# Performance work log

Hardware: AMD Instinct MI355X
Metric: run time of the kernel (lower is better)

The kernel has to match this reference:

```python
import jax, jax.numpy as jnp
import numpy as np

N_NODES = 40000
N_EDGES = 640000
D_IN = 128
D_OUT = 128


def setup_inputs() -> dict:
    key = jax.random.key(0)
    k_feat, k_src, k_dst, k_ws, k_wn = jax.random.split(key, 5)
    feat = jax.random.normal(k_feat, (N_NODES, D_IN), dtype=jnp.float32)
    src = jax.random.randint(k_src, (N_EDGES,), 0, N_NODES, dtype=jnp.int32)
    dst = jax.random.randint(k_dst, (N_EDGES,), 0, N_NODES, dtype=jnp.int32)
    # Glorot-ish init for the two dense layers
    scale = 1.0 / np.sqrt(D_IN)
    W_self = jax.random.normal(k_ws, (D_IN, D_OUT), dtype=jnp.float32) * scale
    W_neigh = jax.random.normal(k_wn, (D_IN, D_OUT), dtype=jnp.float32) * scale
    b_self = jnp.zeros((D_OUT,), dtype=jnp.float32)
    b_neigh = jnp.zeros((D_OUT,), dtype=jnp.float32)
    return {"feat": feat, "src": src, "dst": dst,
            "W_self": W_self, "b_self": b_self,
            "W_neigh": W_neigh, "b_neigh": b_neigh}


def reference(feat, src, dst, W_self, b_self, W_neigh, b_neigh):
    # --- mean aggregation: copy_src('h','m') + mean('m','neigh') ---
    # Gather source features along edges, segment-sum into dst, divide by in-degree.
    msgs = feat[src]  # [E, D_in]
    neigh_sum = jax.ops.segment_sum(msgs, dst, num_segments=N_NODES)  # [N, D_in]
    deg = jax.ops.segment_sum(jnp.ones((src.shape[0],), feat.dtype), dst,
                              num_segments=N_NODES)  # [N]
    # DGL mean reducer yields 0 for nodes with no incoming edges.
    h_neigh = neigh_sum / jnp.maximum(deg, 1.0)[:, None]
    # --- fc_self(h_self) + fc_neigh(h_neigh) ---
    rst = (feat @ W_self + b_self) + (h_neigh @ W_neigh + b_neigh)
    return rst
```

## Files before the change

### kernel.cpp

```cpp
#include <hip/hip_runtime.h>
#include <cstddef>

constexpr int NN  = 40000;
constexpr int NE  = 640000;
constexpr int DIM = 128;
constexpr int CAP = 48;
constexpr int PLANE = NN * 64;

typedef __attribute__((ext_vector_type(8))) short short8;
typedef __attribute__((ext_vector_type(4))) float floatx4;

__device__ __forceinline__ unsigned short f2bf(float x) {
    union { float f; unsigned int i; } v; v.f = x;
    unsigned int u = v.i;
    return (unsigned short)((u + 0x7fffu + ((u >> 16) & 1u)) >> 16);
}
__device__ __forceinline__ float bflo2f(unsigned int u) {
    union { unsigned int i; float f; } v; v.i = u << 16; return v.f;
}
__device__ __forceinline__ float bfhi2f(unsigned int u) {
    union { unsigned int i; float f; } v; v.i = u & 0xffff0000u; return v.f;
}

__global__ __launch_bounds__(256) void k_prep(
    const float* __restrict__ feat, const float* __restrict__ Wself,
    const float* __restrict__ Wneigh, unsigned short* __restrict__ featb,
    unsigned short* __restrict__ Wc, int* __restrict__ cnt)
{
    int b = blockIdx.x, t = threadIdx.x;
    if (b < 2500) {
        int idx8 = b * 256 + t;
        int n  = idx8 >> 4;
        int d0 = (idx8 & 15) << 3;
        const float4* fp =
            reinterpret_cast<const float4*>(feat + (size_t)n * DIM + d0);
        float4 v0 = fp[0], v1 = fp[1];
        unsigned int p0 = (unsigned int)f2bf(v0.x) | ((unsigned int)f2bf(v0.y) << 16);
        unsigned int p1 = (unsigned int)f2bf(v0.z) | ((unsigned int)f2bf(v0.w) << 16);
        unsigned int p2 = (unsigned int)f2bf(v1.x) | ((unsigned int)f2bf(v1.y) << 16);
        unsigned int p3 = (unsigned int)f2bf(v1.z) | ((unsigned int)f2bf(v1.w) << 16);
        int plane = d0 >> 6, off = d0 & 63;
        *reinterpret_cast<uint4*>(
            featb + (size_t)plane * PLANE + (size_t)n * 64 + off) =
            make_uint4(p0, p1, p2, p3);
    } else if (b < 2628) {
        int idx = (b - 2500) * 256 + t;
        int c = idx >> 13, n = (idx >> 6) & 127, kp = idx & 63;
        int k = c * 64 + kp;
        float w = (k < DIM) ? Wself[(size_t)k * DIM + n]
                            : Wneigh[(size_t)(k - DIM) * DIM + n];
        Wc[idx] = f2bf(w);
    } else {
        int i = (b - 2628) * 256 + t;
        if (i < NN) cnt[i] = 0;
    }
}

__global__ __launch_bounds__(256) void k_fill(
    const int* __restrict__ src, const int* __restrict__ dst,
    int* __restrict__ cnt, unsigned short* __restrict__ colf)
{
    int e = blockIdx.x * blockDim.x + threadIdx.x;
    if (e < NE) {
        int d = dst[e];
        int pos = atomicAdd(&cnt[d], 1);
        if (pos < CAP) colf[d * CAP + pos] = (unsigned short)src[e];
    }
}

__global__ __launch_bounds__(256) void k_gather(
    const unsigned int* __restrict__ fb32,
    const int* __restrict__ cnt,
    const unsigned short* __restrict__ colf,
    unsigned int* __restrict__ hnb32)
{
    int gtid = blockIdx.x * blockDim.x + threadIdx.x;
    int n = gtid >> 6;
    if (n >= NN) return;
    int lane = threadIdx.x & 63;

    int deg = cnt[n];
    int m = min(deg, CAP);
    int sv = (lane < m) ? (int)colf[n * CAP + lane] : 0;

    int vb = (lane >> 5) * (NN * 32) + (lane & 31);
    float ax0 = 0.f, ay0 = 0.f, ax1 = 0.f, ay1 = 0.f;
    int i = 0;
    for (; i + 3 < m; i += 4) {
        int s0 = __shfl(sv, i),     s1 = __shfl(sv, i + 1);
        int s2 = __shfl(sv, i + 2), s3 = __shfl(sv, i + 3);
        unsigned int u0 = fb32[vb + s0 * 32];
        unsigned int u1 = fb32[vb + s1 * 32];
        unsigned int u2 = fb32[vb + s2 * 32];
        unsigned int u3 = fb32[vb + s3 * 32];
        ax0 += bflo2f(u0); ay0 += bfhi2f(u0);
        ax1 += bflo2f(u1); ay1 += bfhi2f(u1);
        ax0 += bflo2f(u2); ay0 += bfhi2f(u2);
        ax1 += bflo2f(u3); ay1 += bfhi2f(u3);
    }
    for (; i < m; ++i) {
        int s0 = __shfl(sv, i);
        unsigned int u0 = fb32[vb + s0 * 32];
        ax0 += bflo2f(u0); ay0 += bfhi2f(u0);
    }
    float inv = 1.0f / fmaxf((float)deg, 1.0f);
    float ax = (ax0 + ax1) * inv, ay = (ay0 + ay1) * inv;
    hnb32[vb + n * 32] = (unsigned int)f2bf(ax) | ((unsigned int)f2bf(ay) << 16);
}

__global__ __launch_bounds__(320) void k_gemm(
    const unsigned short* __restrict__ featb,
    const unsigned short* __restrict__ hnb,
    const unsigned short* __restrict__ Wc,
    const float* __restrict__ bself, const float* __restrict__ bneigh,
    float* __restrict__ out)
{
    __shared__ unsigned short As[160 * 64];
    __shared__ unsigned short Bs[128 * 64];

    int t = threadIdx.x;
    int w = t >> 6;
    int lane = t & 63;
    int base_m = blockIdx.x * 160;

    floatx4 acc[2][8];
    #pragma unroll
    for (int a = 0; a < 2; ++a)
        #pragma unroll
        for (int b = 0; b < 8; ++b) acc[a][b] = (floatx4)0.f;

    for (int c = 0; c < 4; ++c) {
        const unsigned short* srcp =
            ((c < 2) ? featb + (size_t)c * PLANE
                     : hnb + (size_t)(c - 2) * PLANE) + (size_t)base_m * 64;
        #pragma unroll
        for (int it = 0; it < 4; ++it) {
            int slot = t + it * 320;
            __builtin_amdgcn_global_load_lds(
                (const __attribute__((address_space(1))) unsigned int*)(srcp + slot * 8),
                (__attribute__((address_space(3))) unsigned int*)(As + slot * 8),
                16, 0, 0);
        }
        if (t < 256) {
            const unsigned short* bp = Wc + (size_t)c * 128 * 64;
            #pragma unroll
            for (int it = 0; it < 4; ++it) {
                int slot = t + it * 256;
                __builtin_amdgcn_global_load_lds(
                    (const __attribute__((address_space(1))) unsigned int*)(bp + slot * 8),
                    (__attribute__((address_space(3))) unsigned int*)(Bs + slot * 8),
                    16, 0, 0);
            }
        }
        __syncthreads();

        #pragma unroll
        for (int s = 0; s < 2; ++s) {
            int koff = s * 32 + (lane >> 4) * 8;
            short8 af[2];
            #pragma unroll
            for (int mt = 0; mt < 2; ++mt) {
                int m = w * 32 + mt * 16 + (lane & 15);
                af[mt] = *reinterpret_cast<const short8*>(As + m * 64 + koff);
            }
            #pragma unroll
            for (int nt = 0; nt < 8; ++nt) {
                int n = nt * 16 + (lane & 15);
                short8 bf = *reinterpret_cast<const short8*>(Bs + n * 64 + koff);
                acc[0][nt] = __builtin_amdgcn_mfma_f32_16x16x32_bf16(
                    af[0], bf, acc[0][nt], 0, 0, 0);
                acc[1][nt] = __builtin_amdgcn_mfma_f32_16x16x32_bf16(
                    af[1], bf, acc[1][nt], 0, 0, 0);
            }
        }
        __syncthreads();
    }

    int colb = lane & 15;
    int quad = lane >> 4;
    #pragma unroll
    for (int nt = 0; nt < 8; ++nt) {
        int col = nt * 16 + colb;
        float bb = bself[col] + bneigh[col];
        #pragma unroll
        for (int mt = 0; mt < 2; ++mt) {
            #pragma unroll
            for (int r = 0; r < 4; ++r) {
                int row = base_m + w * 32 + mt * 16 + quad * 4 + r;
                out[(size_t)row * DIM + col] = acc[mt][nt][r] + bb;
            }
        }
    }
}

extern "C" void kernel_launch(void* const* d_in, const int* in_sizes, int n_in,
                              void* d_out, int out_size, void* d_ws, size_t ws_size,
                              hipStream_t stream)
{
    const float* feat   = (const float*)d_in[0];
    const int*   src    = (const int*)d_in[1];
    const int*   dst    = (const int*)d_in[2];
    const float* Wself  = (const float*)d_in[3];
    const float* bself  = (const float*)d_in[4];
    const float* Wneigh = (const float*)d_in[5];
    const float* bneigh = (const float*)d_in[6];
    float* out = (float*)d_out;

    char* ws = (char*)d_ws;
    unsigned short* featb = (unsigned short*)(ws);
    unsigned short* hnb   = (unsigned short*)(ws + 10240000);
    unsigned short* colf  = (unsigned short*)(ws + 20480000);
    unsigned short* Wc    = (unsigned short*)(ws + 24320000);
    int*            cnt   = (int*)(ws + 24385536);

    k_prep<<<2785, 256, 0, stream>>>(feat, Wself, Wneigh, featb, Wc, cnt);

    k_fill<<<(NE + 255) / 256, 256, 0, stream>>>(src, dst, cnt, colf);

    k_gather<<<(NN * 64) / 256, 256, 0, stream>>>(
        (const unsigned int*)featb, cnt, colf, (unsigned int*)hnb);

    k_gemm<<<NN / 160, 320, 0, stream>>>(featb, hnb, Wc, bself, bneigh, out);
}
```

Measured before the change: 148.7 us.

## Use 32-column bf16 planes, split gather per plane, fuse prep and fill

```diff
diff --git a/kernel.cpp b/kernel.cpp
--- a/kernel.cpp
+++ b/kernel.cpp
@@ -5,7 +5,8 @@
 constexpr int NE  = 640000;
 constexpr int DIM = 128;
 constexpr int CAP = 48;
-constexpr int PLANE = NN * 64;
+constexpr int PLANE32   = NN * 32;
+constexpr int PLANE32_U = NN * 16;
 
 typedef __attribute__((ext_vector_type(8))) short short8;
 typedef __attribute__((ext_vector_type(4))) float floatx4;
@@ -22,10 +23,12 @@
     union { unsigned int i; float f; } v; v.i = u & 0xffff0000u; return v.f;
 }
 
-__global__ __launch_bounds__(256) void k_prep(
+__global__ __launch_bounds__(256) void k_prep_fill(
     const float* __restrict__ feat, const float* __restrict__ Wself,
-    const float* __restrict__ Wneigh, unsigned short* __restrict__ featb,
-    unsigned short* __restrict__ Wc, int* __restrict__ cnt)
+    const float* __restrict__ Wneigh, const int* __restrict__ src,
+    const int* __restrict__ dst, unsigned short* __restrict__ featb,
+    unsigned short* __restrict__ Wc, int* __restrict__ cnt,
+    unsigned short* __restrict__ colf)
 {
     int b = blockIdx.x, t = threadIdx.x;
     if (b < 2500) {
@@ -39,9 +42,9 @@
         unsigned int p1 = (unsigned int)f2bf(v0.z) | ((unsigned int)f2bf(v0.w) << 16);
         unsigned int p2 = (unsigned int)f2bf(v1.x) | ((unsigned int)f2bf(v1.y) << 16);
         unsigned int p3 = (unsigned int)f2bf(v1.z) | ((unsigned int)f2bf(v1.w) << 16);
-        int plane = d0 >> 6, off = d0 & 63;
+        int plane = d0 >> 5, off = d0 & 31;
         *reinterpret_cast<uint4*>(
-            featb + (size_t)plane * PLANE + (size_t)n * 64 + off) =
+            featb + (size_t)plane * PLANE32 + (size_t)n * 32 + off) =
             make_uint4(p0, p1, p2, p3);
     } else if (b < 2628) {
         int idx = (b - 2500) * 256 + t;
@@ -51,17 +54,7 @@
                             : Wneigh[(size_t)(k - DIM) * DIM + n];
         Wc[idx] = f2bf(w);
     } else {
-        int i = (b - 2628) * 256 + t;
-        if (i < NN) cnt[i] = 0;
-    }
-}
-
-__global__ __launch_bounds__(256) void k_fill(
-    const int* __restrict__ src, const int* __restrict__ dst,
-    int* __restrict__ cnt, unsigned short* __restrict__ colf)
-{
-    int e = blockIdx.x * blockDim.x + threadIdx.x;
-    if (e < NE) {
+        int e = (b - 2628) * 256 + t;
         int d = dst[e];
         int pos = atomicAdd(&cnt[d], 1);
         if (pos < CAP) colf[d * CAP + pos] = (unsigned short)src[e];
@@ -74,38 +67,35 @@
     const unsigned short* __restrict__ colf,
     unsigned int* __restrict__ hnb32)
 {
-    int gtid = blockIdx.x * blockDim.x + threadIdx.x;
-    int n = gtid >> 6;
-    if (n >= NN) return;
+    int g = blockIdx.x;
+    int p = g & 3;
+    int n = ((g >> 2) << 2) + (threadIdx.x >> 6);
     int lane = threadIdx.x & 63;
+    int j = lane >> 4;
+    int u = lane & 15;
 
     int deg = cnt[n];
     int m = min(deg, CAP);
     int sv = (lane < m) ? (int)colf[n * CAP + lane] : 0;
 
-    int vb = (lane >> 5) * (NN * 32) + (lane & 31);
-    float ax0 = 0.f, ay0 = 0.f, ax1 = 0.f, ay1 = 0.f;
-    int i = 0;
-    for (; i + 3 < m; i += 4) {
-        int s0 = __shfl(sv, i),     s1 = __shfl(sv, i + 1);
-        int s2 = __shfl(sv, i + 2), s3 = __shfl(sv, i + 3);
-        unsigned int u0 = fb32[vb + s0 * 32];
-        unsigned int u1 = fb32[vb + s1 * 32];
-        unsigned int u2 = fb32[vb + s2 * 32];
-        unsigned int u3 = fb32[vb + s3 * 32];
-        ax0 += bflo2f(u0); ay0 += bfhi2f(u0);
-        ax1 += bflo2f(u1); ay1 += bfhi2f(u1);
-        ax0 += bflo2f(u2); ay0 += bfhi2f(u2);
-        ax1 += bflo2f(u3); ay1 += bfhi2f(u3);
-    }
-    for (; i < m; ++i) {
-        int s0 = __shfl(sv, i);
-        unsigned int u0 = fb32[vb + s0 * 32];
-        ax0 += bflo2f(u0); ay0 += bfhi2f(u0);
-    }
-    float inv = 1.0f / fmaxf((float)deg, 1.0f);
-    float ax = (ax0 + ax1) * inv, ay = (ay0 + ay1) * inv;
-    hnb32[vb + n * 32] = (unsigned int)f2bf(ax) | ((unsigned int)f2bf(ay) << 16);
+    const unsigned int* pb = fb32 + (size_t)p * PLANE32_U;
+    float ax = 0.f, ay = 0.f;
+    for (int i = 0; i < m; i += 8) {
+        int i0 = i + j, i1 = i + 4 + j;
+        int s0 = __shfl(sv, i0);
+        int s1 = __shfl(sv, i1);
+        unsigned int v0 = pb[s0 * 16 + u];
+        unsigned int v1 = pb[s1 * 16 + u];
+        if (i0 < m) { ax += bflo2f(v0); ay += bfhi2f(v0); }
+        if (i1 < m) { ax += bflo2f(v1); ay += bfhi2f(v1); }
+    }
+    ax += __shfl_xor(ax, 16); ay += __shfl_xor(ay, 16);
+    ax += __shfl_xor(ax, 32); ay += __shfl_xor(ay, 32);
+    if (lane < 16) {
+        float inv = 1.0f / fmaxf((float)deg, 1.0f);
+        hnb32[(size_t)p * PLANE32_U + (size_t)n * 16 + u] =
+            (unsigned int)f2bf(ax * inv) | ((unsigned int)f2bf(ay * inv) << 16);
+    }
 }
 
 __global__ __launch_bounds__(320) void k_gemm(
@@ -115,62 +105,57 @@
     const float* __restrict__ bself, const float* __restrict__ bneigh,
     float* __restrict__ out)
 {
-    __shared__ unsigned short As[160 * 64];
-    __shared__ unsigned short Bs[128 * 64];
+    __shared__ __align__(16) unsigned short As[80 * 64];
+    __shared__ __align__(16) unsigned short Bs[128 * 64];
 
     int t = threadIdx.x;
     int w = t >> 6;
     int lane = t & 63;
-    int base_m = blockIdx.x * 160;
-
-    floatx4 acc[2][8];
+    int base_m = blockIdx.x * 80;
+
+    floatx4 acc[8];
     #pragma unroll
-    for (int a = 0; a < 2; ++a)
+    for (int i = 0; i < 8; ++i) acc[i] = (floatx4)0.f;
+
+    for (int c = 0; c < 4; ++c) {
+        const unsigned short* sp = (c < 2) ? featb : hnb;
+        int cc = c & 1;
         #pragma unroll
-        for (int b = 0; b < 8; ++b) acc[a][b] = (floatx4)0.f;
-
-    for (int c = 0; c < 4; ++c) {
-        const unsigned short* srcp =
-            ((c < 2) ? featb + (size_t)c * PLANE
-                     : hnb + (size_t)(c - 2) * PLANE) + (size_t)base_m * 64;
-        #pragma unroll
-        for (int it = 0; it < 4; ++it) {
-            int slot = t + it * 320;
+        for (int it = 0; it < 2; ++it) {
+            int s = t + it * 320;
+            int m = s >> 3, q = s & 7;
+            const unsigned short* sa =
+                sp + (size_t)(2 * cc + (q >> 2)) * PLANE32
+                   + (size_t)(base_m + m) * 32 + (q & 3) * 8;
             __builtin_amdgcn_global_load_lds(
-                (const __attribute__((address_space(1))) unsigned int*)(srcp + slot * 8),
-                (__attribute__((address_space(3))) unsigned int*)(As + slot * 8),
+                (const __attribute__((address_space(1))) unsigned int*)sa,
+                (__attribute__((address_space(3))) unsigned int*)(As + s * 8),
                 16, 0, 0);
         }
         if (t < 256) {
-            const unsigned short* bp = Wc + (size_t)c * 128 * 64;
+            const unsigned short* bp = Wc + (size_t)c * 8192;
             #pragma unroll
             for (int it = 0; it < 4; ++it) {
-                int slot = t + it * 256;
+                int s = t + it * 256;
                 __builtin_amdgcn_global_load_lds(
-                    (const __attribute__((address_space(1))) unsigned int*)(bp + slot * 8),
-                    (__attribute__((address_space(3))) unsigned int*)(Bs + slot * 8),
+                    (const __attribute__((address_space(1))) unsigned int*)(bp + s * 8),
+                    (__attribute__((address_space(3))) unsigned int*)(Bs + s * 8),
                     16, 0, 0);
             }
         }
         __syncthreads();
 
         #pragma unroll
-        for (int s = 0; s < 2; ++s) {
-            int koff = s * 32 + (lane >> 4) * 8;
-            short8 af[2];
-            #pragma unroll
-            for (int mt = 0; mt < 2; ++mt) {
-                int m = w * 32 + mt * 16 + (lane & 15);
-                af[mt] = *reinterpret_cast<const short8*>(As + m * 64 + koff);
-            }
+        for (int sstep = 0; sstep < 2; ++sstep) {
+            int koff = sstep * 32 + (lane >> 4) * 8;
+            short8 af = *reinterpret_cast<const short8*>(
+                As + (w * 16 + (lane & 15)) * 64 + koff);
             #pragma unroll
             for (int nt = 0; nt < 8; ++nt) {
-                int n = nt * 16 + (lane & 15);
-                short8 bf = *reinterpret_cast<const short8*>(Bs + n * 64 + koff);
-                acc[0][nt] = __builtin_amdgcn_mfma_f32_16x16x32_bf16(
-                    af[0], bf, acc[0][nt], 0, 0, 0);
-                acc[1][nt] = __builtin_amdgcn_mfma_f32_16x16x32_bf16(
-                    af[1], bf, acc[1][nt], 0, 0, 0);
+                short8 bf = *reinterpret_cast<const short8*>(
+                    Bs + (nt * 16 + (lane & 15)) * 64 + koff);
+                acc[nt] = __builtin_amdgcn_mfma_f32_16x16x32_bf16(
+                    af, bf, acc[nt], 0, 0, 0);
             }
         }
         __syncthreads();
@@ -183,12 +168,9 @@
         int col = nt * 16 + colb;
         float bb = bself[col] + bneigh[col];
         #pragma unroll
-        for (int mt = 0; mt < 2; ++mt) {
-            #pragma unroll
-            for (int r = 0; r < 4; ++r) {
-                int row = base_m + w * 32 + mt * 16 + quad * 4 + r;
-                out[(size_t)row * DIM + col] = acc[mt][nt][r] + bb;
-            }
+        for (int r = 0; r < 4; ++r) {
+            int row = base_m + w * 16 + quad * 4 + r;
+            out[(size_t)row * DIM + col] = acc[nt][r] + bb;
         }
     }
 }
@@ -213,12 +195,13 @@
     unsigned short* Wc    = (unsigned short*)(ws + 24320000);
     int*            cnt   = (int*)(ws + 24385536);
 
-    k_prep<<<2785, 256, 0, stream>>>(feat, Wself, Wneigh, featb, Wc, cnt);
-
-    k_fill<<<(NE + 255) / 256, 256, 0, stream>>>(src, dst, cnt, colf);
-
-    k_gather<<<(NN * 64) / 256, 256, 0, stream>>>(
+    hipMemsetAsync(cnt, 0, NN * sizeof(int), stream);
+
+    k_prep_fill<<<5128, 256, 0, stream>>>(
+        feat, Wself, Wneigh, src, dst, featb, Wc, cnt, colf);
+
+    k_gather<<<40000, 256, 0, stream>>>(
         (const unsigned int*)featb, cnt, colf, (unsigned int*)hnb);
 
-    k_gemm<<<NN / 160, 320, 0, stream>>>(featb, hnb, Wc, bself, bneigh, out);
-}
+    k_gemm<<<500, 320, 0, stream>>>(featb, hnb, Wc, bself, bneigh, out);
+}
```

Measured after the change: 184.6 us. +24.2%, slower.
